# Kernel tuning notes

Hardware: AMD Instinct MI355X
Metric: run time of the kernel (lower is better)

The kernel has to match this reference:

```python
import jax, jax.numpy as jnp
import numpy as np

B, C, H, W = 2, 64, 512, 512
HEADS = 4
EPS = 1e-12  # F.normalize eps


def setup_inputs() -> dict:
    key = jax.random.key(0)
    ks = jax.random.split(key, 7)
    s = 0.02
    return {
        "x": jax.random.normal(ks[0], (B, C, H, W), jnp.float32),
        "Wq": jax.random.normal(ks[1], (C, C), jnp.float32) * s,
        "Wk": jax.random.normal(ks[2], (C, C), jnp.float32) * s,
        "Wv": jax.random.normal(ks[3], (C, C), jnp.float32) * s,
        "Wp": jax.random.normal(ks[4], (C, C), jnp.float32) * s,
        "bp": jax.random.normal(ks[5], (C,), jnp.float32) * s,
        "rescale": jnp.ones((HEADS, 1, 1), jnp.float32),
    }


def reference(x, Wq, Wk, Wv, Wp, bp, rescale):
    b, c, h, w = x.shape
    n = h * w
    d = c // HEADS
    xf = x.reshape(b, c, n)  # 1x1 conv == channel matmul on flattened spatial

    def conv1x1(Wt):
        return jnp.einsum('oc,bcn->bon', Wt, xf)

    # torch: permute->reshape(b,n,c)->split heads->transpose == reshape conv out to (b,heads,d,n)
    q = conv1x1(Wq).reshape(b, HEADS, d, n)
    k = conv1x1(Wk).reshape(b, HEADS, d, n)
    v = conv1x1(Wv).reshape(b, HEADS, d, n)

    def l2norm(t):  # F.normalize(p=2, dim=-1)
        nrm = jnp.sqrt(jnp.sum(t * t, axis=-1, keepdims=True))
        return t / jnp.maximum(nrm, EPS)

    q = l2norm(q)
    k = l2norm(k)

    attn = jnp.einsum('bhdn,bhen->bhde', k, q)  # (b, heads, d, d) tiny matrix
    attn = attn * rescale  # rescale broadcasts (heads,1,1)
    attn = jax.nn.softmax(attn, axis=-1)

    o = jnp.einsum('bhde,bhen->bhdn', attn, v).reshape(b, c, n)
    out = jnp.einsum('oc,bcn->bon', Wp, o) + bp[None, :, None] + xf  # proj + residual
    return out.reshape(b, c, h, w)
```

## Files before the change

### kernel.cpp

```cpp
#include <hip/hip_runtime.h>
#include <math.h>

#define C 64
#define NHEADS 4
#define DH 16
#define NN 262144
#define NB 2
#define PB 512
#define NT 2
#define EPS 1e-12f

typedef __attribute__((ext_vector_type(8))) short short8v;
typedef __attribute__((ext_vector_type(8))) unsigned short ushort8v;
typedef __attribute__((ext_vector_type(4))) float f32x4;

static __device__ __forceinline__ unsigned short f2bf(float f) {
  union { float f; unsigned int u; } v; v.f = f;
  unsigned int r = v.u + 0x7fffu + ((v.u >> 16) & 1u);
  return (unsigned short)(r >> 16);
}

__global__ __launch_bounds__(256, 2) void gram_kernel(const float* __restrict__ x,
                                                      float* __restrict__ Gc) {
  __shared__ unsigned short xs[C * 256];
  const int b = blockIdx.y;
  const int chunk = blockIdx.x;
  const float* xb = x + (size_t)b * C * NN;
  const int t = threadIdx.x;
  const int w = t >> 6, l = t & 63;
  const int lrow = l & 15, lhi = l >> 4;

  const int gA0 = (w >> 1) * 2, gA1 = gA0 + 1;
  const int gB0 = (w & 1) * 2,  gB1 = gB0 + 1;
  const int cA0 = gA0 * 16 + lrow, cA1 = gA1 * 16 + lrow;
  const int cB0 = gB0 * 16 + lrow, cB1 = gB1 * 16 + lrow;

  f32x4 acc0 = {0.f,0.f,0.f,0.f}, acc1 = {0.f,0.f,0.f,0.f};
  f32x4 acc2 = {0.f,0.f,0.f,0.f}, acc3 = {0.f,0.f,0.f,0.f};

  for (int tile = 0; tile < NT; ++tile) {
    const int j0 = (chunk * NT + tile) * 256;
    __syncthreads();
#pragma unroll
    for (int i = 0; i < 8; ++i) {
      const int oi = i * 256 + t;
      const int c = oi >> 5, oct = oi & 31;
      const float* src = xb + (size_t)c * NN + j0 + oct * 8;
      const float4 v0 = *reinterpret_cast<const float4*>(src);
      const float4 v1 = *reinterpret_cast<const float4*>(src + 4);
      ushort8v pk;
      pk[0] = f2bf(v0.x); pk[1] = f2bf(v0.y); pk[2] = f2bf(v0.z); pk[3] = f2bf(v0.w);
      pk[4] = f2bf(v1.x); pk[5] = f2bf(v1.y); pk[6] = f2bf(v1.z); pk[7] = f2bf(v1.w);
      *reinterpret_cast<ushort8v*>(&xs[c * 256 + ((oct ^ (c & 7)) << 3)]) = pk;
    }
    __syncthreads();
#pragma unroll
    for (int s = 0; s < 8; ++s) {
      const int o = s * 4 + lhi;
      const short8v fA0 = *reinterpret_cast<const short8v*>(&xs[cA0 * 256 + ((o ^ (cA0 & 7)) << 3)]);
      const short8v fA1 = *reinterpret_cast<const short8v*>(&xs[cA1 * 256 + ((o ^ (cA1 & 7)) << 3)]);
      const short8v fB0 = *reinterpret_cast<const short8v*>(&xs[cB0 * 256 + ((o ^ (cB0 & 7)) << 3)]);
      const short8v fB1 = *reinterpret_cast<const short8v*>(&xs[cB1 * 256 + ((o ^ (cB1 & 7)) << 3)]);
      acc0 = __builtin_amdgcn_mfma_f32_16x16x32_bf16(fA0, fB0, acc0, 0, 0, 0);
      acc1 = __builtin_amdgcn_mfma_f32_16x16x32_bf16(fA0, fB1, acc1, 0, 0, 0);
      acc2 = __builtin_amdgcn_mfma_f32_16x16x32_bf16(fA1, fB0, acc2, 0, 0, 0);
      acc3 = __builtin_amdgcn_mfma_f32_16x16x32_bf16(fA1, fB1, acc3, 0, 0, 0);
    }
  }
  float* g = Gc + ((size_t)b * PB + chunk) * 4096;
#pragma unroll
  for (int r = 0; r < 4; ++r) {
    const int row = lhi * 4 + r;
    g[(gA0 * 16 + row) * 64 + gB0 * 16 + lrow] = acc0[r];
    g[(gA0 * 16 + row) * 64 + gB1 * 16 + lrow] = acc1[r];
    g[(gA1 * 16 + row) * 64 + gB0 * 16 + lrow] = acc2[r];
    g[(gA1 * 16 + row) * 64 + gB1 * 16 + lrow] = acc3[r];
  }
}

__global__ __launch_bounds__(256) void reduce_kernel(const float* __restrict__ Gc,
                                                     float* __restrict__ G) {
  __shared__ float s[4][64];
  const int b = blockIdx.y;
  const int g = blockIdx.x;
  const int t = threadIdx.x;
  const int e = g * 64 + (t & 63);
  const int chunk = t >> 6;
  float sum = 0.f;
  for (int p = chunk; p < PB; p += 4)
    sum += Gc[((size_t)b * PB + p) * 4096 + e];
  s[chunk][t & 63] = sum;
  __syncthreads();
  if (t < 64) G[(size_t)b * 4096 + g * 64 + t] = s[0][t] + s[1][t] + s[2][t] + s[3][t];
}

__global__ __launch_bounds__(256) void attn_kernel(const float* __restrict__ G,
    const float* __restrict__ Wq, const float* __restrict__ Wk,
    const float* __restrict__ Wv, const float* __restrict__ Wp,
    const float* __restrict__ rescale, unsigned short* __restrict__ Ebf) {
  __shared__ float Gs[4096], GQt[4096], GKt[4096], T[4096];
  __shared__ float attnw[64][DH];
  __shared__ float nq[64], nk[64];
  const int b = blockIdx.x;
  const int t = threadIdx.x;

  for (int i = t; i < 4096; i += 256) Gs[i] = G[(size_t)b * 4096 + i];
  __syncthreads();
  for (int i = t; i < 4096; i += 256) {
    const int c = i >> 6, e = i & 63;
    float sq_ = 0.f, sk_ = 0.f;
    for (int c2 = 0; c2 < 64; ++c2) {
      const float g = Gs[c * 64 + c2];
      sq_ += g * Wq[e * 64 + c2];
      sk_ += g * Wk[e * 64 + c2];
    }
    GQt[c * 64 + e] = sq_;
    GKt[c * 64 + e] = sk_;
  }
  __syncthreads();
  if (t < 64) {
    float s = 0.f;
    for (int c2 = 0; c2 < 64; ++c2) s += Wq[t * 64 + c2] * GQt[c2 * 64 + t];
    nq[t] = sqrtf(fmaxf(s, 0.f));
  } else if (t < 128) {
    const int d = t - 64;
    float s = 0.f;
    for (int c2 = 0; c2 < 64; ++c2) s += Wk[d * 64 + c2] * GKt[c2 * 64 + d];
    nk[d] = sqrtf(fmaxf(s, 0.f));
  }
  __syncthreads();
  if (t < 64) {
    const int h = t >> 4;
    const float rs = rescale[h];
    const float nkd = fmaxf(nk[t], EPS);
    float logits[DH];
    float mx = -1e30f;
    for (int ee = 0; ee < DH; ++ee) {
      const int e = h * DH + ee;
      float num = 0.f;
      for (int c2 = 0; c2 < 64; ++c2) num += Wk[t * 64 + c2] * GQt[c2 * 64 + e];
      const float l = num / (nkd * fmaxf(nq[e], EPS)) * rs;
      logits[ee] = l;
      mx = fmaxf(mx, l);
    }
    float sum = 0.f;
    for (int ee = 0; ee < DH; ++ee) { const float p = expf(logits[ee] - mx); logits[ee] = p; sum += p; }
    const float inv = 1.f / sum;
    for (int ee = 0; ee < DH; ++ee) attnw[t][ee] = logits[ee] * inv;
  }
  __syncthreads();
  for (int i = t; i < 4096; i += 256) {
    const int r = i >> 6, c = i & 63;
    const int h = r >> 4;
    float s = 0.f;
    for (int e = 0; e < DH; ++e) s += attnw[r][e] * Wv[(h * DH + e) * 64 + c];
    T[i] = s;
  }
  __syncthreads();
  for (int i = t; i < 4096; i += 256) {
    const int r = i >> 6, c = i & 63;
    float s = (r == c) ? 1.f : 0.f;
    for (int m = 0; m < 64; ++m) s += Wp[r * 64 + m] * T[m * 64 + c];
    Ebf[(size_t)b * 4096 + i] = f2bf(s);
  }
}

__global__ __launch_bounds__(256, 4) void apply_B(const float* __restrict__ x,
    const unsigned short* __restrict__ Ebf, const float* __restrict__ bp,
    float* __restrict__ out) {
  const int b = blockIdx.y;
  const float* xb = x + (size_t)b * C * NN;
  float* ob = out + (size_t)b * C * NN;
  const int t = threadIdx.x;
  const int w = t >> 6, l = t & 63;
  const int lrow = l & 15, lhi = l >> 4;

  short8v ef[4][2];
  const unsigned short* eb = Ebf + (size_t)b * 4096;
#pragma unroll
  for (int ot = 0; ot < 4; ++ot)
#pragma unroll
    for (int ks = 0; ks < 2; ++ks)
      ef[ot][ks] = *reinterpret_cast<const short8v*>(eb + (ot * 16 + lrow) * 64 + ks * 32 + lhi * 8);

  float bias[4];
#pragma unroll
  for (int ot = 0; ot < 4; ++ot) bias[ot] = bp[ot * 16 + lrow];

  const int gw = blockIdx.x * 4 + w;

#pragma unroll 1
  for (int ci = 0; ci < 4; ++ci) {
    const int n0 = (gw * 4 + ci) * 32;
    float xv[32];
#pragma unroll
    for (int nn = 0; nn < 2; ++nn) {
      const int n = n0 + nn * 16 + lrow;
#pragma unroll
      for (int ks = 0; ks < 2; ++ks) {
        const float* src = xb + (size_t)(ks * 32 + lhi * 8) * NN + n;
#pragma unroll
        for (int j = 0; j < 8; ++j)
          xv[nn * 16 + ks * 8 + j] = src[(size_t)j * NN];
      }
    }
    short8v xf[2][2];
#pragma unroll
    for (int nn = 0; nn < 2; ++nn)
#pragma unroll
      for (int ks = 0; ks < 2; ++ks) {
        ushort8v pk;
#pragma unroll
        for (int j = 0; j < 8; ++j) pk[j] = f2bf(xv[nn * 16 + ks * 8 + j]);
        xf[nn][ks] = *reinterpret_cast<short8v*>(&pk);
      }
    f32x4 acc[4][2];
#pragma unroll
    for (int ot = 0; ot < 4; ++ot)
#pragma unroll
      for (int nn = 0; nn < 2; ++nn) acc[ot][nn] = (f32x4){0.f, 0.f, 0.f, 0.f};
#pragma unroll
    for (int nn = 0; nn < 2; ++nn)
#pragma unroll
      for (int ks = 0; ks < 2; ++ks)
#pragma unroll
        for (int ot = 0; ot < 4; ++ot)
          acc[ot][nn] = __builtin_amdgcn_mfma_f32_16x16x32_bf16(xf[nn][ks], ef[ot][ks], acc[ot][nn], 0, 0, 0);
#pragma unroll
    for (int ot = 0; ot < 4; ++ot) {
      const int o = ot * 16 + lrow;
#pragma unroll
      for (int nn = 0; nn < 2; ++nn) {
        float4 o4;
        o4.x = acc[ot][nn][0] + bias[ot];
        o4.y = acc[ot][nn][1] + bias[ot];
        o4.z = acc[ot][nn][2] + bias[ot];
        o4.w = acc[ot][nn][3] + bias[ot];
        *reinterpret_cast<float4*>(&ob[(size_t)o * NN + n0 + nn * 16 + lhi * 4]) = o4;
      }
    }
  }
}

extern "C" void kernel_launch(void* const* d_in, const int* in_sizes, int n_in,
                              void* d_out, int out_size, void* d_ws, size_t ws_size,
                              hipStream_t stream) {
  const float* x       = (const float*)d_in[0];
  const float* Wq      = (const float*)d_in[1];
  const float* Wk      = (const float*)d_in[2];
  const float* Wv      = (const float*)d_in[3];
  const float* Wp      = (const float*)d_in[4];
  const float* bp      = (const float*)d_in[5];
  const float* rescale = (const float*)d_in[6];
  float* out = (float*)d_out;

  float* Gc = out;
  float* G  = (float*)d_ws;
  unsigned short* Ebf = (unsigned short*)(G + (size_t)NB * 4096);

  gram_kernel<<<dim3(PB, NB), dim3(256), 0, stream>>>(x, Gc);
  reduce_kernel<<<dim3(64, NB), dim3(256), 0, stream>>>(Gc, G);
  attn_kernel<<<dim3(NB), dim3(256), 0, stream>>>(G, Wq, Wk, Wv, Wp, rescale, Ebf);
  apply_B<<<dim3(512, NB), dim3(256), 0, stream>>>(x, Ebf, bp, out);
}
```

Baseline: 158.2 us.

## Load gram MFMA operands directly from global memory, drop LDS staging

The gram kernel no longer stages a bf16 tile of x in shared memory. Each wave now loads its own MFMA operand rows straight from global memory into registers and converts them there. This removes the LDS writes and reads and both block barriers, and raises the occupancy hint to 4 blocks per SM. In exchange, waves reload overlapping channel rows, which increases L1/L2 traffic, and the per-lane global access pattern is less coalesced.

```diff
diff --git a/kernel.cpp b/kernel.cpp
--- a/kernel.cpp
+++ b/kernel.cpp
@@ -20,9 +20,15 @@
   return (unsigned short)(r >> 16);
 }
 
-__global__ __launch_bounds__(256, 2) void gram_kernel(const float* __restrict__ x,
+static __device__ __forceinline__ short8v pack8(float4 v0, float4 v1) {
+  ushort8v pk;
+  pk[0] = f2bf(v0.x); pk[1] = f2bf(v0.y); pk[2] = f2bf(v0.z); pk[3] = f2bf(v0.w);
+  pk[4] = f2bf(v1.x); pk[5] = f2bf(v1.y); pk[6] = f2bf(v1.z); pk[7] = f2bf(v1.w);
+  return *reinterpret_cast<short8v*>(&pk);
+}
+
+__global__ __launch_bounds__(256, 4) void gram_kernel(const float* __restrict__ x,
                                                       float* __restrict__ Gc) {
-  __shared__ unsigned short xs[C * 256];
   const int b = blockIdx.y;
   const int chunk = blockIdx.x;
   const float* xb = x + (size_t)b * C * NN;
@@ -32,35 +38,32 @@
 
   const int gA0 = (w >> 1) * 2, gA1 = gA0 + 1;
   const int gB0 = (w & 1) * 2,  gB1 = gB0 + 1;
-  const int cA0 = gA0 * 16 + lrow, cA1 = gA1 * 16 + lrow;
-  const int cB0 = gB0 * 16 + lrow, cB1 = gB1 * 16 + lrow;
+  const float* rA0 = xb + (size_t)(gA0 * 16 + lrow) * NN;
+  const float* rA1 = xb + (size_t)(gA1 * 16 + lrow) * NN;
+  const float* rB0 = xb + (size_t)(gB0 * 16 + lrow) * NN;
+  const float* rB1 = xb + (size_t)(gB1 * 16 + lrow) * NN;
 
   f32x4 acc0 = {0.f,0.f,0.f,0.f}, acc1 = {0.f,0.f,0.f,0.f};
   f32x4 acc2 = {0.f,0.f,0.f,0.f}, acc3 = {0.f,0.f,0.f,0.f};
 
+#pragma unroll 1
   for (int tile = 0; tile < NT; ++tile) {
     const int j0 = (chunk * NT + tile) * 256;
-    __syncthreads();
-#pragma unroll
-    for (int i = 0; i < 8; ++i) {
-      const int oi = i * 256 + t;
-      const int c = oi >> 5, oct = oi & 31;
-      const float* src = xb + (size_t)c * NN + j0 + oct * 8;
-      const float4 v0 = *reinterpret_cast<const float4*>(src);
-      const float4 v1 = *reinterpret_cast<const float4*>(src + 4);
-      ushort8v pk;
-      pk[0] = f2bf(v0.x); pk[1] = f2bf(v0.y); pk[2] = f2bf(v0.z); pk[3] = f2bf(v0.w);
-      pk[4] = f2bf(v1.x); pk[5] = f2bf(v1.y); pk[6] = f2bf(v1.z); pk[7] = f2bf(v1.w);
-      *reinterpret_cast<ushort8v*>(&xs[c * 256 + ((oct ^ (c & 7)) << 3)]) = pk;
-    }
-    __syncthreads();
-#pragma unroll
+#pragma unroll 2
     for (int s = 0; s < 8; ++s) {
-      const int o = s * 4 + lhi;
-      const short8v fA0 = *reinterpret_cast<const short8v*>(&xs[cA0 * 256 + ((o ^ (cA0 & 7)) << 3)]);
-      const short8v fA1 = *reinterpret_cast<const short8v*>(&xs[cA1 * 256 + ((o ^ (cA1 & 7)) << 3)]);
-      const short8v fB0 = *reinterpret_cast<const short8v*>(&xs[cB0 * 256 + ((o ^ (cB0 & 7)) << 3)]);
-      const short8v fB1 = *reinterpret_cast<const short8v*>(&xs[cB1 * 256 + ((o ^ (cB1 & 7)) << 3)]);
+      const int off = j0 + s * 32 + lhi * 8;
+      const float4 a00 = *reinterpret_cast<const float4*>(rA0 + off);
+      const float4 a01 = *reinterpret_cast<const float4*>(rA0 + off + 4);
+      const float4 a10 = *reinterpret_cast<const float4*>(rA1 + off);
+      const float4 a11 = *reinterpret_cast<const float4*>(rA1 + off + 4);
+      const float4 b00 = *reinterpret_cast<const float4*>(rB0 + off);
+      const float4 b01 = *reinterpret_cast<const float4*>(rB0 + off + 4);
+      const float4 b10 = *reinterpret_cast<const float4*>(rB1 + off);
+      const float4 b11 = *reinterpret_cast<const float4*>(rB1 + off + 4);
+      const short8v fA0 = pack8(a00, a01);
+      const short8v fA1 = pack8(a10, a11);
+      const short8v fB0 = pack8(b00, b01);
+      const short8v fB1 = pack8(b10, b11);
       acc0 = __builtin_amdgcn_mfma_f32_16x16x32_bf16(fA0, fB0, acc0, 0, 0, 0);
       acc1 = __builtin_amdgcn_mfma_f32_16x16x32_bf16(fA0, fB1, acc1, 0, 0, 0);
       acc2 = __builtin_amdgcn_mfma_f32_16x16x32_bf16(fA1, fB0, acc2, 0, 0, 0);
```

New measurement: 197.4 us. 24.8% more time.
